# Kernel optimization log

Hardware: AMD Instinct MI355X
Metric: run time of the kernel (lower is better)

## Reference

```python
import math
import jax, jax.numpy as jnp
import numpy as np

B, S, D, H = 2, 2048, 1024, 16
HD = D // H  # 64


def setup_inputs() -> dict:
    key = jax.random.key(0)
    k = jax.random.split(key, 8)
    x = jax.random.normal(k[0], (B, S, D), dtype=jnp.float32)
    # RoPE tables: inv_freq over half dim, emb = concat(freqs, freqs)
    inv_freq = 1.0 / (10000.0 ** (jnp.arange(0, HD, 2, dtype=jnp.float32) / HD))
    pos = jnp.arange(S, dtype=jnp.float32)
    freqs = pos[:, None] * inv_freq[None, :]            # [S, HD/2]
    emb = jnp.concatenate([freqs, freqs], axis=-1)      # [S, HD]
    cos = jnp.cos(emb)[:, None, :]                      # [S, 1, HD] broadcasts over [B,S,H,HD]
    sin = jnp.sin(emb)[:, None, :]
    # causal additive mask [1, 1, S, S]
    neg = jnp.finfo(jnp.float32).min
    mask = jnp.where(jnp.tril(jnp.ones((S, S), dtype=bool)), 0.0, neg)[None, None]
    scale = 0.02
    wq = jax.random.normal(k[1], (D, D), dtype=jnp.float32) * scale
    wk = jax.random.normal(k[2], (D, D), dtype=jnp.float32) * scale
    wv = jax.random.normal(k[3], (D, D), dtype=jnp.float32) * scale
    wo = jax.random.normal(k[4], (D, D), dtype=jnp.float32) * scale
    return {"x": x, "cos": cos, "sin": sin, "mask": mask,
            "wq": wq, "wk": wk, "wv": wv, "wo": wo}


def rotate_half(t):
    t1, t2 = t[..., : t.shape[-1] // 2], t[..., t.shape[-1] // 2:]
    return jnp.concatenate([-t2, t1], axis=-1)


def reference(x, cos, sin, mask, wq, wk, wv, wo):
    b, s, d = x.shape
    # torch nn.Linear: y = x @ W^T  (W is [out, in])
    q = (x @ wq.T).reshape(b, s, H, HD)
    kk = (x @ wk.T).reshape(b, s, H, HD)
    v = (x @ wv.T).reshape(b, s, H, HD)
    q = q * cos + rotate_half(q) * sin
    kk = kk * cos + rotate_half(kk) * sin
    q = q.transpose(0, 2, 1, 3)   # [b, h, s, hd]
    kk = kk.transpose(0, 2, 1, 3)
    v = v.transpose(0, 2, 1, 3)
    scores = jnp.einsum('bhqd,bhkd->bhqk', q, kk) / math.sqrt(HD)
    scores = scores + mask
    probs = jax.nn.softmax(scores.astype(jnp.float32), axis=-1).astype(q.dtype)
    out = jnp.einsum('bhqk,bhkd->bhqd', probs, v)
    out = out.transpose(0, 2, 1, 3).reshape(b, s, d)
    return out @ wo.T
```

## Files before the change

### kernel.cpp

```cpp
#include <hip/hip_runtime.h>
#include <hip/hip_bf16.h>

typedef __hip_bfloat16 bf16;
typedef unsigned short u16;
typedef __attribute__((ext_vector_type(8))) short short8;
typedef __attribute__((ext_vector_type(4))) float floatx4;

constexpr int B_ = 2, S_ = 2048, D_ = 1024, H_ = 16, HD_ = 64;
constexpr int QT = 64, KT = 64, PAD = 72;
constexpr int NQT = S_ / QT;
constexpr int GK = 1024, BK = 64;

__device__ inline float b2f(u16 u) {
    union { unsigned int i; float f; } v; v.i = ((unsigned int)u) << 16; return v.f;
}
__device__ inline u16 f2b(float f) {
    bf16 h = __float2bfloat16(f); return *(u16*)&h;
}

__device__ inline void gl16(const u16* g, u16* l) {
    __builtin_amdgcn_global_load_lds(
        (const __attribute__((address_space(1))) unsigned int*)g,
        (__attribute__((address_space(3))) unsigned int*)l, 16, 0, 0);
}

__global__ __launch_bounds__(256) void cvt_kernel(
    const float* __restrict__ x,  const float* __restrict__ wq,
    const float* __restrict__ wk, const float* __restrict__ wv,
    const float* __restrict__ wo,
    u16* __restrict__ Xb, u16* __restrict__ Wb)
{
    const size_t c = (size_t)blockIdx.x * 256 + threadIdx.x;
    const float* src; u16* dst; size_t off;
    if (c < (size_t)(1 << 19)) { src = x; dst = Xb; off = c; }
    else {
        const size_t w = c - (1 << 19);
        const int wi = (int)(w >> 17);
        off = w & ((1 << 17) - 1);
        src = (wi == 0) ? wq : (wi == 1) ? wk : (wi == 2) ? wv : wo;
        dst = Wb + ((size_t)wi << 20);
    }
    const float4 a = *(const float4*)(src + off * 8);
    const float4 b = *(const float4*)(src + off * 8 + 4);
    ushort4 u0; u0.x = f2b(a.x); u0.y = f2b(a.y); u0.z = f2b(a.z); u0.w = f2b(a.w);
    ushort4 u1; u1.x = f2b(b.x); u1.y = f2b(b.y); u1.z = f2b(b.z); u1.w = f2b(b.w);
    *(ushort4*)(dst + off * 8)     = u0;
    *(ushort4*)(dst + off * 8 + 4) = u1;
}

template <typename TC, int SCATTER, int ROPE>
__global__ __launch_bounds__(256) void gemm_async(
    const u16* __restrict__ A, const u16* __restrict__ Wb,
    const float* __restrict__ cosp, const float* __restrict__ sinp,
    TC* __restrict__ C0, TC* __restrict__ C1, TC* __restrict__ C2, int N)
{
    const u16* W = Wb + ((size_t)blockIdx.z << 20);
    TC*        C = (blockIdx.z == 0) ? C0 : (blockIdx.z == 1 ? C1 : C2);

    __shared__ __align__(16) u16 As[128 * BK];
    __shared__ __align__(16) u16 Bs[128 * BK];

    const int tid  = threadIdx.x;
    const int wave = tid >> 6, lane = tid & 63;
    const int quad = lane >> 4, l16 = lane & 15;
    const int wm = wave >> 1, wn = wave & 1;
    const int m0 = blockIdx.y * 128, n0 = blockIdx.x * 128;

    const int srl = lane >> 3;
    const int sc  = (lane & 7) ^ srl;

    floatx4 acc[4][4] = {};

    for (int k0 = 0; k0 < GK; k0 += BK) {
        __syncthreads();
#pragma unroll
        for (int j = 0; j < 4; ++j) {
            const int rb = wave * 32 + j * 8;
            gl16(A + (size_t)(m0 + rb + srl) * GK + k0 + sc * 8, &As[rb * BK]);
            gl16(W + (size_t)(n0 + rb + srl) * GK + k0 + sc * 8, &Bs[rb * BK]);
        }
        __syncthreads();

#pragma unroll
        for (int ks = 0; ks < 2; ++ks) {
            short8 af[4], bfr[4];
#pragma unroll
            for (int mt = 0; mt < 4; ++mt) {
                const int R = wm * 64 + mt * 16 + l16;
                af[mt] = *(const short8*)&As[R * BK + (((ks * 4 + quad) ^ (l16 & 7)) * 8)];
            }
#pragma unroll
            for (int nt = 0; nt < 4; ++nt) {
                const int R = wn * 64 + nt * 16 + l16;
                bfr[nt] = *(const short8*)&Bs[R * BK + (((ks * 4 + quad) ^ (l16 & 7)) * 8)];
            }
#pragma unroll
            for (int mt = 0; mt < 4; ++mt)
#pragma unroll
                for (int nt = 0; nt < 4; ++nt)
                    acc[mt][nt] = __builtin_amdgcn_mfma_f32_16x16x32_bf16(
                        af[mt], bfr[nt], acc[mt][nt], 0, 0, 0);
        }
    }

    if (ROPE && blockIdx.z < 2) {
        const float scale = (blockIdx.z == 0) ? 0.125f * 1.44269504f : 1.0f;
        const int h = (n0 + wn * 64) >> 6;
#pragma unroll
        for (int mt = 0; mt < 4; ++mt)
#pragma unroll
            for (int r = 0; r < 4; ++r) {
                const int m = m0 + wm * 64 + mt * 16 + quad * 4 + r;
                const int b = m >> 11, s = m & (S_ - 1);
                const size_t base = ((size_t)(b * H_ + h) * S_ + s) << 6;
#pragma unroll
                for (int np = 0; np < 2; ++np) {
                    const int d = np * 16 + l16;
                    const float c1 = cosp[s * HD_ + d];
                    const float s1 = sinp[s * HD_ + d];
                    const float c2 = cosp[s * HD_ + d + 32];
                    const float s2 = sinp[s * HD_ + d + 32];
                    const float q0 = acc[mt][np][r], q1 = acc[mt][np + 2][r];
                    ((bf16*)C)[base + d]      = __float2bfloat16((q0 * c1 - q1 * s1) * scale);
                    ((bf16*)C)[base + d + 32] = __float2bfloat16((q1 * c2 + q0 * s2) * scale);
                }
            }
    } else if (SCATTER) {
        const int h = (n0 + wn * 64) >> 6;
#pragma unroll
        for (int mt = 0; mt < 4; ++mt)
#pragma unroll
            for (int nt = 0; nt < 4; ++nt)
#pragma unroll
                for (int r = 0; r < 4; ++r) {
                    const int m = m0 + wm * 64 + mt * 16 + quad * 4 + r;
                    const int b = m >> 11, s = m & (S_ - 1);
                    const int hd = nt * 16 + l16;
                    ((bf16*)C)[(((size_t)(b * H_ + h) * S_ + s) << 6) + hd] =
                        __float2bfloat16(acc[mt][nt][r]);
                }
    } else {
#pragma unroll
        for (int mt = 0; mt < 4; ++mt)
#pragma unroll
            for (int nt = 0; nt < 4; ++nt)
#pragma unroll
                for (int r = 0; r < 4; ++r) {
                    const int m = m0 + wm * 64 + mt * 16 + quad * 4 + r;
                    const int n = n0 + wn * 64 + nt * 16 + l16;
                    ((float*)C)[(size_t)m * N + n] = acc[mt][nt][r];
                }
    }
}

__global__ __launch_bounds__(256) void vt_kernel(
    const u16* __restrict__ V, u16* __restrict__ Vt)
{
    __shared__ u16 T[HD_ * 72];
    const int s0 = blockIdx.x * 64;
    const int bh = blockIdx.z * H_ + blockIdx.y;
    const int tid = threadIdx.x;
    const int r = tid >> 2, c = (tid & 3) * 16;

    const u16* src = V + ((size_t)bh * S_ + s0 + r) * HD_ + c;
    const short8 v0 = *(const short8*)src;
    const short8 v1 = *(const short8*)(src + 8);
#pragma unroll
    for (int j = 0; j < 8; ++j) {
        T[(c + j)     * 72 + r] = (u16)v0[j];
        T[(c + 8 + j) * 72 + r] = (u16)v1[j];
    }
    __syncthreads();
    const short8 o0 = *(const short8*)&T[r * 72 + c];
    const short8 o1 = *(const short8*)&T[r * 72 + c + 8];
    u16* dst = Vt + ((size_t)bh * HD_ + r) * S_ + s0 + c;
    *(short8*)dst       = o0;
    *(short8*)(dst + 8) = o1;
}

__global__ __launch_bounds__(256) void fa_kernel(
    const u16* __restrict__ Qg, const u16* __restrict__ Kg, const u16* __restrict__ Vt,
    bf16* __restrict__ Og)
{
    __shared__ __align__(16) u16 Kt[2][KT * PAD];
    __shared__ __align__(16) u16 Vs[2][HD_ * PAD];
    __shared__ __align__(16) u16 Pt[4 * 16 * PAD];

    const int flat = blockIdx.x;
    const int bx = flat >> 5;
    const int bh = flat & 31;
    const int b  = bh >> 4, h = bh & 15;
    const int tid  = threadIdx.x;
    const int wave = tid >> 6, lane = tid & 63;
    const int quad = lane >> 4, l16 = lane & 15;
    const int srow = tid >> 2, scol = (tid & 3) * 16;

    const short8 ones = {16256,16256,16256,16256,16256,16256,16256,16256};

    for (int half = 0; half < 2; ++half) {
        const int qt = half ? (NQT - 1 - bx) : bx;
        const int qb = qt * QT;

        const u16* qrow = Qg + ((size_t)bh * S_ + qb + wave * 16 + l16) * HD_;
        const short8 aq0 = *(const short8*)(qrow + quad * 8);
        const short8 aq1 = *(const short8*)(qrow + 32 + quad * 8);

        floatx4 oacc[4] = {{0,0,0,0},{0,0,0,0},{0,0,0,0},{0,0,0,0}};
        floatx4 lacc = {0,0,0,0};

        __syncthreads();
        {
            const u16* kp = Kg + ((size_t)bh * S_ + srow) * HD_ + scol;
            *(short8*)&Kt[0][srow * PAD + scol]     = *(const short8*)kp;
            *(short8*)&Kt[0][srow * PAD + scol + 8] = *(const short8*)(kp + 8);
            const u16* vp = Vt + ((size_t)bh * HD_ + srow) * S_ + scol;
            *(short8*)&Vs[0][srow * PAD + scol]     = *(const short8*)vp;
            *(short8*)&Vs[0][srow * PAD + scol + 8] = *(const short8*)(vp + 8);
        }
        __syncthreads();

        for (int it = 0; it <= qt; ++it) {
            const int  cur = it & 1;
            const bool pf  = (it < qt);
            short8 nk0, nk1, nv0, nv1;
            if (pf) {
                const int kb = (it + 1) * KT;
                const u16* kp = Kg + ((size_t)bh * S_ + kb + srow) * HD_ + scol;
                nk0 = *(const short8*)kp; nk1 = *(const short8*)(kp + 8);
                const u16* vp = Vt + ((size_t)bh * HD_ + srow) * S_ + kb + scol;
                nv0 = *(const short8*)vp; nv1 = *(const short8*)(vp + 8);
            }

            floatx4 sacc[4] = {{0,0,0,0},{0,0,0,0},{0,0,0,0},{0,0,0,0}};
#pragma unroll
            for (int nt = 0; nt < 4; ++nt) {
                const short8 bk0 = *(const short8*)&Kt[cur][(nt * 16 + l16) * PAD + quad * 8];
                const short8 bk1 = *(const short8*)&Kt[cur][(nt * 16 + l16) * PAD + 32 + quad * 8];
                sacc[nt] = __builtin_amdgcn_mfma_f32_16x16x32_bf16(aq0, bk0, sacc[nt], 0, 0, 0);
                sacc[nt] = __builtin_amdgcn_mfma_f32_16x16x32_bf16(aq1, bk1, sacc[nt], 0, 0, 0);
            }

            if (it == qt) {
#pragma unroll
                for (int r = 0; r < 4; ++r) {
                    const int qr = wave * 16 + quad * 4 + r;
#pragma unroll
                    for (int nt = 0; nt < 4; ++nt)
                        if (nt * 16 + l16 > qr) sacc[nt][r] = -1.0e38f;
                }
            }

#pragma unroll
            for (int nt = 0; nt < 4; ++nt)
#pragma unroll
                for (int r = 0; r < 4; ++r)
                    Pt[(wave * 16 + quad * 4 + r) * PAD + nt * 16 + l16] =
                        f2b(__builtin_amdgcn_exp2f(sacc[nt][r]));

            const short8 ap0 = *(const short8*)&Pt[(wave * 16 + l16) * PAD + quad * 8];
            const short8 ap1 = *(const short8*)&Pt[(wave * 16 + l16) * PAD + 32 + quad * 8];

#pragma unroll
            for (int nt = 0; nt < 4; ++nt) {
                const short8 bv0 = *(const short8*)&Vs[cur][(nt * 16 + l16) * PAD + quad * 8];
                const short8 bv1 = *(const short8*)&Vs[cur][(nt * 16 + l16) * PAD + 32 + quad * 8];
                oacc[nt] = __builtin_amdgcn_mfma_f32_16x16x32_bf16(ap0, bv0, oacc[nt], 0, 0, 0);
                oacc[nt] = __builtin_amdgcn_mfma_f32_16x16x32_bf16(ap1, bv1, oacc[nt], 0, 0, 0);
            }
            lacc = __builtin_amdgcn_mfma_f32_16x16x32_bf16(ap0, ones, lacc, 0, 0, 0);
            lacc = __builtin_amdgcn_mfma_f32_16x16x32_bf16(ap1, ones, lacc, 0, 0, 0);

            if (pf) {
                const int nb = cur ^ 1;
                *(short8*)&Kt[nb][srow * PAD + scol]     = nk0;
                *(short8*)&Kt[nb][srow * PAD + scol + 8] = nk1;
                *(short8*)&Vs[nb][srow * PAD + scol]     = nv0;
                *(short8*)&Vs[nb][srow * PAD + scol + 8] = nv1;
            }
            __syncthreads();
        }

        float inv[4];
#pragma unroll
        for (int r = 0; r < 4; ++r) inv[r] = 1.0f / lacc[r];
#pragma unroll
        for (int nt = 0; nt < 4; ++nt)
#pragma unroll
            for (int r = 0; r < 4; ++r) {
                const int qg = qb + wave * 16 + quad * 4 + r;
                Og[((size_t)(b * S_ + qg)) * D_ + h * HD_ + nt * 16 + l16] =
                    __float2bfloat16(oacc[nt][r] * inv[r]);
            }
    }
}

extern "C" void kernel_launch(void* const* d_in, const int* in_sizes, int n_in,
                              void* d_out, int out_size, void* d_ws, size_t ws_size,
                              hipStream_t stream)
{
    const float* x    = (const float*)d_in[0];
    const float* cosp = (const float*)d_in[1];
    const float* sinp = (const float*)d_in[2];
    const float* wq   = (const float*)d_in[4];
    const float* wk   = (const float*)d_in[5];
    const float* wv   = (const float*)d_in[6];
    const float* wo   = (const float*)d_in[7];
    float* out = (float*)d_out;

    u16* w0 = (u16*)d_ws;
    const size_t NE = (size_t)B_ * S_ * D_;
    u16* Qb  = w0;
    u16* Kb  = w0 + NE;
    u16* Vb  = w0 + 2 * NE;
    u16* Vtb = w0 + 3 * NE;
    u16* Xb  = w0 + 4 * NE;
    u16* Wb  = w0 + 5 * NE;
    u16* Ab  = Xb;
    u16* Wob = Wb + 3 * (1 << 20);

    cvt_kernel<<<4096, 256, 0, stream>>>(x, wq, wk, wv, wo, Xb, Wb);

    gemm_async<bf16, 1, 1><<<dim3(D_ / 128, (B_ * S_) / 128, 3), 256, 0, stream>>>(
        Xb, Wb, cosp, sinp, (bf16*)Qb, (bf16*)Kb, (bf16*)Vb, D_);

    vt_kernel<<<dim3(S_ / 64, H_, B_), 256, 0, stream>>>(Vb, Vtb);

    fa_kernel<<<dim3((NQT / 2) * 32, 1, 1), 256, 0, stream>>>(Qb, Kb, Vtb, (bf16*)Ab);

    gemm_async<float, 0, 0><<<dim3(D_ / 128, (B_ * S_) / 128, 1), 256, 0, stream>>>(
        Ab, Wob, cosp, sinp, out, out, out, D_);
}
```

Before: 211.5 us.

## Remap GEMM blocks per XCD, shrink output-projection tile, transpose attention MFMAs

The GEMM now runs on a flat 1D grid whose block index is remapped so that tiles sharing A rows sit on the same XCD, which aims at better L2 reuse. The output projection uses a narrower 128x64 tile so it launches 512 blocks instead of 256 and fills more CUs. The attention kernel swaps the MFMA operand order so each lane holds one query row's values: the row sum is taken with shuffles instead of an extra ones-MFMA, and P and O are written as packed 4-element vectors. This cuts MFMA work and scattered stores, but the mapping is hardcoded to these shapes and to 8 XCDs.

```diff
diff --git a/kernel.cpp b/kernel.cpp
--- a/kernel.cpp
+++ b/kernel.cpp
@@ -48,28 +48,43 @@
     *(ushort4*)(dst + off * 8 + 4) = u1;
 }
 
-template <typename TC, int SCATTER, int ROPE>
+template <typename TC, int SCATTER, int ROPE, int BN>
 __global__ __launch_bounds__(256) void gemm_async(
     const u16* __restrict__ A, const u16* __restrict__ Wb,
     const float* __restrict__ cosp, const float* __restrict__ sinp,
     TC* __restrict__ C0, TC* __restrict__ C1, TC* __restrict__ C2, int N)
 {
-    const u16* W = Wb + ((size_t)blockIdx.z << 20);
-    TC*        C = (blockIdx.z == 0) ? C0 : (blockIdx.z == 1 ? C1 : C2);
+    constexpr int NT = BN / 32;
+
+    int x, y, z;
+    {
+        const int xcd = blockIdx.x & 7, idx = blockIdx.x >> 3;
+        y = (xcd & 3) * 8 + (idx & 7);
+        if (BN == 128) {
+            const int xz = (xcd >> 2) * 12 + (idx >> 3);
+            x = xz & 7; z = xz >> 3;
+        } else {
+            x = (xcd >> 2) * 8 + (idx >> 3);
+            z = 0;
+        }
+    }
+
+    const u16* W = Wb + ((size_t)z << 20);
+    TC*        C = (z == 0) ? C0 : (z == 1 ? C1 : C2);
 
     __shared__ __align__(16) u16 As[128 * BK];
-    __shared__ __align__(16) u16 Bs[128 * BK];
+    __shared__ __align__(16) u16 Bs[BN * BK];
 
     const int tid  = threadIdx.x;
     const int wave = tid >> 6, lane = tid & 63;
     const int quad = lane >> 4, l16 = lane & 15;
     const int wm = wave >> 1, wn = wave & 1;
-    const int m0 = blockIdx.y * 128, n0 = blockIdx.x * 128;
+    const int m0 = y * 128, n0 = x * BN;
 
     const int srl = lane >> 3;
     const int sc  = (lane & 7) ^ srl;
 
-    floatx4 acc[4][4] = {};
+    floatx4 acc[4][NT] = {};
 
     for (int k0 = 0; k0 < GK; k0 += BK) {
         __syncthreads();
@@ -77,34 +92,38 @@
         for (int j = 0; j < 4; ++j) {
             const int rb = wave * 32 + j * 8;
             gl16(A + (size_t)(m0 + rb + srl) * GK + k0 + sc * 8, &As[rb * BK]);
+        }
+#pragma unroll
+        for (int j = 0; j < BN / 32; ++j) {
+            const int rb = wave * (BN / 4) + j * 8;
             gl16(W + (size_t)(n0 + rb + srl) * GK + k0 + sc * 8, &Bs[rb * BK]);
         }
         __syncthreads();
 
 #pragma unroll
         for (int ks = 0; ks < 2; ++ks) {
-            short8 af[4], bfr[4];
+            short8 af[4], bfr[NT];
 #pragma unroll
             for (int mt = 0; mt < 4; ++mt) {
                 const int R = wm * 64 + mt * 16 + l16;
                 af[mt] = *(const short8*)&As[R * BK + (((ks * 4 + quad) ^ (l16 & 7)) * 8)];
             }
 #pragma unroll
-            for (int nt = 0; nt < 4; ++nt) {
-                const int R = wn * 64 + nt * 16 + l16;
+            for (int nt = 0; nt < NT; ++nt) {
+                const int R = wn * (BN / 2) + nt * 16 + l16;
                 bfr[nt] = *(const short8*)&Bs[R * BK + (((ks * 4 + quad) ^ (l16 & 7)) * 8)];
             }
 #pragma unroll
             for (int mt = 0; mt < 4; ++mt)
 #pragma unroll
-                for (int nt = 0; nt < 4; ++nt)
+                for (int nt = 0; nt < NT; ++nt)
                     acc[mt][nt] = __builtin_amdgcn_mfma_f32_16x16x32_bf16(
                         af[mt], bfr[nt], acc[mt][nt], 0, 0, 0);
         }
     }
 
-    if (ROPE && blockIdx.z < 2) {
-        const float scale = (blockIdx.z == 0) ? 0.125f * 1.44269504f : 1.0f;
+    if (ROPE && z < 2) {
+        const float scale = (z == 0) ? 0.125f * 1.44269504f : 1.0f;
         const int h = (n0 + wn * 64) >> 6;
 #pragma unroll
         for (int mt = 0; mt < 4; ++mt)
@@ -130,7 +149,7 @@
 #pragma unroll
         for (int mt = 0; mt < 4; ++mt)
 #pragma unroll
-            for (int nt = 0; nt < 4; ++nt)
+            for (int nt = 0; nt < NT; ++nt)
 #pragma unroll
                 for (int r = 0; r < 4; ++r) {
                     const int m = m0 + wm * 64 + mt * 16 + quad * 4 + r;
@@ -143,11 +162,11 @@
 #pragma unroll
         for (int mt = 0; mt < 4; ++mt)
 #pragma unroll
-            for (int nt = 0; nt < 4; ++nt)
+            for (int nt = 0; nt < NT; ++nt)
 #pragma unroll
                 for (int r = 0; r < 4; ++r) {
                     const int m = m0 + wm * 64 + mt * 16 + quad * 4 + r;
-                    const int n = n0 + wn * 64 + nt * 16 + l16;
+                    const int n = n0 + wn * (BN / 2) + nt * 16 + l16;
                     ((float*)C)[(size_t)m * N + n] = acc[mt][nt][r];
                 }
     }
@@ -195,8 +214,6 @@
     const int quad = lane >> 4, l16 = lane & 15;
     const int srow = tid >> 2, scol = (tid & 3) * 16;
 
-    const short8 ones = {16256,16256,16256,16256,16256,16256,16256,16256};
-
     for (int half = 0; half < 2; ++half) {
         const int qt = half ? (NQT - 1 - bx) : bx;
         const int qb = qt * QT;
@@ -206,7 +223,7 @@
         const short8 aq1 = *(const short8*)(qrow + 32 + quad * 8);
 
         floatx4 oacc[4] = {{0,0,0,0},{0,0,0,0},{0,0,0,0},{0,0,0,0}};
-        floatx4 lacc = {0,0,0,0};
+        float lsum = 0.f;
 
         __syncthreads();
         {
@@ -233,42 +250,47 @@
 
             floatx4 sacc[4] = {{0,0,0,0},{0,0,0,0},{0,0,0,0},{0,0,0,0}};
 #pragma unroll
-            for (int nt = 0; nt < 4; ++nt) {
-                const short8 bk0 = *(const short8*)&Kt[cur][(nt * 16 + l16) * PAD + quad * 8];
-                const short8 bk1 = *(const short8*)&Kt[cur][(nt * 16 + l16) * PAD + 32 + quad * 8];
-                sacc[nt] = __builtin_amdgcn_mfma_f32_16x16x32_bf16(aq0, bk0, sacc[nt], 0, 0, 0);
-                sacc[nt] = __builtin_amdgcn_mfma_f32_16x16x32_bf16(aq1, bk1, sacc[nt], 0, 0, 0);
+            for (int kt = 0; kt < 4; ++kt) {
+                const short8 bk0 = *(const short8*)&Kt[cur][(kt * 16 + l16) * PAD + quad * 8];
+                const short8 bk1 = *(const short8*)&Kt[cur][(kt * 16 + l16) * PAD + 32 + quad * 8];
+                sacc[kt] = __builtin_amdgcn_mfma_f32_16x16x32_bf16(bk0, aq0, sacc[kt], 0, 0, 0);
+                sacc[kt] = __builtin_amdgcn_mfma_f32_16x16x32_bf16(bk1, aq1, sacc[kt], 0, 0, 0);
             }
 
             if (it == qt) {
-#pragma unroll
-                for (int r = 0; r < 4; ++r) {
-                    const int qr = wave * 16 + quad * 4 + r;
-#pragma unroll
-                    for (int nt = 0; nt < 4; ++nt)
-                        if (nt * 16 + l16 > qr) sacc[nt][r] = -1.0e38f;
-                }
-            }
-
-#pragma unroll
-            for (int nt = 0; nt < 4; ++nt)
-#pragma unroll
-                for (int r = 0; r < 4; ++r)
-                    Pt[(wave * 16 + quad * 4 + r) * PAD + nt * 16 + l16] =
-                        f2b(__builtin_amdgcn_exp2f(sacc[nt][r]));
+                const int ql = wave * 16 + l16;
+#pragma unroll
+                for (int kt = 0; kt < 4; ++kt)
+#pragma unroll
+                    for (int r = 0; r < 4; ++r)
+                        if (kt * 16 + quad * 4 + r > ql) sacc[kt][r] = -1.0e38f;
+            }
+
+            float rs = 0.f;
+#pragma unroll
+            for (int kt = 0; kt < 4; ++kt) {
+                const float e0 = __builtin_amdgcn_exp2f(sacc[kt][0]);
+                const float e1 = __builtin_amdgcn_exp2f(sacc[kt][1]);
+                const float e2 = __builtin_amdgcn_exp2f(sacc[kt][2]);
+                const float e3 = __builtin_amdgcn_exp2f(sacc[kt][3]);
+                rs += (e0 + e1) + (e2 + e3);
+                ushort4 pk; pk.x = f2b(e0); pk.y = f2b(e1); pk.z = f2b(e2); pk.w = f2b(e3);
+                *(ushort4*)&Pt[(wave * 16 + l16) * PAD + kt * 16 + quad * 4] = pk;
+            }
+            rs += __shfl_xor(rs, 16);
+            rs += __shfl_xor(rs, 32);
+            lsum += rs;
 
             const short8 ap0 = *(const short8*)&Pt[(wave * 16 + l16) * PAD + quad * 8];
             const short8 ap1 = *(const short8*)&Pt[(wave * 16 + l16) * PAD + 32 + quad * 8];
 
 #pragma unroll
-            for (int nt = 0; nt < 4; ++nt) {
-                const short8 bv0 = *(const short8*)&Vs[cur][(nt * 16 + l16) * PAD + quad * 8];
-                const short8 bv1 = *(const short8*)&Vs[cur][(nt * 16 + l16) * PAD + 32 + quad * 8];
-                oacc[nt] = __builtin_amdgcn_mfma_f32_16x16x32_bf16(ap0, bv0, oacc[nt], 0, 0, 0);
-                oacc[nt] = __builtin_amdgcn_mfma_f32_16x16x32_bf16(ap1, bv1, oacc[nt], 0, 0, 0);
-            }
-            lacc = __builtin_amdgcn_mfma_f32_16x16x32_bf16(ap0, ones, lacc, 0, 0, 0);
-            lacc = __builtin_amdgcn_mfma_f32_16x16x32_bf16(ap1, ones, lacc, 0, 0, 0);
+            for (int dt = 0; dt < 4; ++dt) {
+                const short8 bv0 = *(const short8*)&Vs[cur][(dt * 16 + l16) * PAD + quad * 8];
+                const short8 bv1 = *(const short8*)&Vs[cur][(dt * 16 + l16) * PAD + 32 + quad * 8];
+                oacc[dt] = __builtin_amdgcn_mfma_f32_16x16x32_bf16(bv0, ap0, oacc[dt], 0, 0, 0);
+                oacc[dt] = __builtin_amdgcn_mfma_f32_16x16x32_bf16(bv1, ap1, oacc[dt], 0, 0, 0);
+            }
 
             if (pf) {
                 const int nb = cur ^ 1;
@@ -280,17 +302,17 @@
             __syncthreads();
         }
 
-        float inv[4];
-#pragma unroll
-        for (int r = 0; r < 4; ++r) inv[r] = 1.0f / lacc[r];
-#pragma unroll
-        for (int nt = 0; nt < 4; ++nt)
-#pragma unroll
-            for (int r = 0; r < 4; ++r) {
-                const int qg = qb + wave * 16 + quad * 4 + r;
-                Og[((size_t)(b * S_ + qg)) * D_ + h * HD_ + nt * 16 + l16] =
-                    __float2bfloat16(oacc[nt][r] * inv[r]);
-            }
+        const float inv = 1.0f / lsum;
+        bf16* orow = Og + ((size_t)(b * S_ + qb + wave * 16 + l16)) * D_ + h * HD_;
+#pragma unroll
+        for (int dt = 0; dt < 4; ++dt) {
+            ushort4 pk;
+            pk.x = f2b(oacc[dt][0] * inv);
+            pk.y = f2b(oacc[dt][1] * inv);
+            pk.z = f2b(oacc[dt][2] * inv);
+            pk.w = f2b(oacc[dt][3] * inv);
+            *(ushort4*)((u16*)orow + dt * 16 + quad * 4) = pk;
+        }
     }
 }
 
@@ -320,13 +342,13 @@
 
     cvt_kernel<<<4096, 256, 0, stream>>>(x, wq, wk, wv, wo, Xb, Wb);
 
-    gemm_async<bf16, 1, 1><<<dim3(D_ / 128, (B_ * S_) / 128, 3), 256, 0, stream>>>(
+    gemm_async<bf16, 1, 1, 128><<<768, 256, 0, stream>>>(
         Xb, Wb, cosp, sinp, (bf16*)Qb, (bf16*)Kb, (bf16*)Vb, D_);
 
     vt_kernel<<<dim3(S_ / 64, H_, B_), 256, 0, stream>>>(Vb, Vtb);
 
     fa_kernel<<<dim3((NQT / 2) * 32, 1, 1), 256, 0, stream>>>(Qb, Kb, Vtb, (bf16*)Ab);
 
-    gemm_async<float, 0, 0><<<dim3(D_ / 128, (B_ * S_) / 128, 1), 256, 0, stream>>>(
+    gemm_async<float, 0, 0, 64><<<512, 256, 0, stream>>>(
         Ab, Wob, cosp, sinp, out, out, out, D_);
 }
```

Result: faster. 201.5 us (-4.7%).
